# Optimization experiments

Measured on AMD Instinct MI355X. Metric: run time of the kernel, lower is better.

The kernel has to match this reference:

```python
import jax, jax.numpy as jnp
import numpy as np

EPS = 1e-5  # torch BatchNorm2d default


def _conv5x5(x, w, b):
    # x: [N,1,H,W], w: [1,1,5,5], b: [1]; stride 1, padding 2 (SAME)
    out = jax.lax.conv_general_dilated(
        x, w, window_strides=(1, 1), padding=((2, 2), (2, 2)),
        dimension_numbers=("NCHW", "OIHW", "NCHW"))
    return out + b[None, :, None, None]


def _batchnorm(x, gamma, beta):
    # training-mode BatchNorm2d: per-channel batch stats over (N,H,W), biased var
    mean = jnp.mean(x, axis=(0, 2, 3), keepdims=True)
    var = jnp.mean(jnp.square(x - mean), axis=(0, 2, 3), keepdims=True)
    xhat = (x - mean) * jax.lax.rsqrt(var + EPS)
    return xhat * gamma[None, :, None, None] + beta[None, :, None, None]


def _shrinkage(x, lumdb):
    return x + 0.5 * (jnp.sqrt(jnp.square(x - lumdb) + 1.0)
                      - jnp.sqrt(jnp.square(x + lumdb) + 1.0))


def setup_inputs() -> dict:
    key = jax.random.key(0)
    k1, k2, k3 = jax.random.split(key, 3)
    y = jax.random.normal(k1, (64, 1, 512, 512), dtype=jnp.float32)
    # kaiming-uniform-ish init for a 1x1x5x5 conv
    fan_in = 25.0
    bound = 1.0 / np.sqrt(fan_in)
    conv_w = jax.random.uniform(k2, (1, 1, 5, 5), jnp.float32, -bound, bound)
    conv_b = jax.random.uniform(k3, (1,), jnp.float32, -bound, bound)
    gamma = jnp.ones((1,), jnp.float32)
    beta = jnp.zeros((1,), jnp.float32)
    lambd = jnp.array([2.0, 1.0, 0.0], jnp.float32)
    return {"y": y, "conv_w": conv_w, "conv_b": conv_b,
            "gamma": gamma, "beta": beta, "lambd": lambd}


def reference(y, conv_w, conv_b, gamma, beta, lambd):
    x_k = y
    # unrolled LISTA iteration 1
    x = _batchnorm(_conv5x5(x_k, conv_w, conv_b), gamma, beta)
    x = _shrinkage(x, lambd[0])
    o12 = _batchnorm(_conv5x5(x, conv_w, conv_b), gamma, beta)
    x = _batchnorm(_conv5x5(x_k, conv_w, conv_b), gamma, beta)
    # iteration 2
    x = _shrinkage(o12 + x, lambd[1])
    o22 = _batchnorm(_conv5x5(x, conv_w, conv_b), gamma, beta)
    x = _batchnorm(_conv5x5(x_k, conv_w, conv_b), gamma, beta)
    # iteration 3
    x = _shrinkage(o22 + x, lambd[2])
    return x
```

## Files before the change

### kernel.cpp

```cpp
#include <hip/hip_runtime.h>
#include <math.h>

#define HH 512
#define WW 512
#define NTOT (64u*512u*512u)
#define NBLK 1024
#define TS 128
#define TROWS 132
#define TCH 18
#define TPIT 152
#define NTASK (TROWS*TCH)
#define NITER 10

typedef __attribute__((ext_vector_type(8))) short short8;
typedef __attribute__((ext_vector_type(4))) float f32x4;

__device__ __forceinline__ float fsqrtf(float x) { return __builtin_amdgcn_sqrtf(x); }

__device__ __forceinline__ float shrinkf(float x, float l) {
    float a = x - l, b = x + l;
    return x + 0.5f * (fsqrtf(__builtin_fmaf(a, a, 1.f)) - fsqrtf(__builtin_fmaf(b, b, 1.f)));
}

__device__ __forceinline__ float bf2f(unsigned int u) {
    union { unsigned int i; float f; } cv;
    cv.i = u << 16;
    return cv.f;
}
__device__ __forceinline__ float lo2f(unsigned int p) {
    union { unsigned int i; float f; } cv; cv.i = p << 16; return cv.f;
}
__device__ __forceinline__ float hi2f(unsigned int p) {
    union { unsigned int i; float f; } cv; cv.i = p & 0xffff0000u; return cv.f;
}

__device__ __forceinline__ unsigned int cvtpk(float lo, float hi) {
    unsigned int r;
    asm("v_cvt_pk_bf16_f32 %0, %1, %2" : "=v"(r) : "v"(lo), "v"(hi));
    return r;
}

__device__ __forceinline__ void bf8(uint4 u, float* f) {
    f[0] = bf2f(u.x & 0xffffu); f[1] = bf2f(u.x >> 16);
    f[2] = bf2f(u.y & 0xffffu); f[3] = bf2f(u.y >> 16);
    f[4] = bf2f(u.z & 0xffffu); f[5] = bf2f(u.z >> 16);
    f[6] = bf2f(u.w & 0xffffu); f[7] = bf2f(u.w >> 16);
}

template <int MODE, bool OBF>
__global__ __launch_bounds__(256, 4) void conv_k(
    const float* __restrict__ yin,
    const unsigned short* __restrict__ t1,
    const unsigned short* __restrict__ t2,
    unsigned short* __restrict__ outbf,
    float* __restrict__ outf32,
    const float* __restrict__ wgt,
    const float* __restrict__ bias,
    const float* __restrict__ stats,
    const float* __restrict__ lambd,
    float* __restrict__ partials)
{
    __shared__ unsigned short tile[TROWS * TPIT];

    const int tid = threadIdx.x;
    const int by = blockIdx.y * TS;
    const int bx = blockIdx.x * TS;
    const size_t ibase = (size_t)blockIdx.z * (HH * WW);

    float s1 = 0.f, h1 = 0.f, s2v = 0.f, h2 = 0.f, lam = 0.f;
    if constexpr (MODE == 1) { s1 = stats[0]; h1 = stats[1]; lam = lambd[0]; }
    if constexpr (MODE == 2) {
        s1 = stats[0]; h1 = stats[1]; s2v = stats[2]; h2 = stats[3]; lam = lambd[1];
    }

    float wloc[25];
#pragma unroll
    for (int i = 0; i < 25; i++) wloc[i] = wgt[i];

    const int lane = tid & 63;
    const int lm = lane & 15;
    const int kb = lane >> 4;
    const int basei = kb * 8 - lm - 6;
    short8 bfr[5];
#pragma unroll
    for (int ky = 0; ky < 5; ky++) {
        unsigned pkw[4];
#pragma unroll
        for (int jj = 0; jj < 4; jj++) {
            float v0 = 0.f, v1 = 0.f;
            const int i0 = basei + 2 * jj, i1 = i0 + 1;
#pragma unroll
            for (int t = 0; t < 5; t++) {
                if (i0 == t) v0 = wloc[ky * 5 + t];
                if (i1 == t) v1 = wloc[ky * 5 + t];
            }
            pkw[jj] = cvtpk(v0, v1);
        }
        union { unsigned u[4]; short8 s; } cv;
        cv.u[0] = pkw[0]; cv.u[1] = pkw[1]; cv.u[2] = pkw[2]; cv.u[3] = pkw[3];
        bfr[ky] = cv.s;
    }

    auto loadT = [&](int task, uint4& A, uint4& B) {
        A = make_uint4(0u,0u,0u,0u); B = make_uint4(0u,0u,0u,0u);
        const int row = task / TCH;
        const int ch  = task - row * TCH;
        const int gy  = by + row - 2;
        const int gx0 = bx + ch * 8 - 8;
        if (task < NTASK && gy >= 0 && gy < HH && gx0 >= 0 && gx0 <= WW - 8) {
            const size_t g = ibase + (size_t)gy * WW + gx0;
            if constexpr (MODE == 0) {
                A = *(const uint4*)(yin + g);
                B = *(const uint4*)(yin + g + 4);
            } else if constexpr (MODE == 1) {
                A = *(const uint4*)(t1 + g);
            } else {
                A = *(const uint4*)(t1 + g);
                B = *(const uint4*)(t2 + g);
            }
        }
    };

    auto procT = [&](int task, uint4 A, uint4 B) {
        const int row = task / TCH;
        const int ch  = task - row * TCH;
        uint4 pk = make_uint4(0u,0u,0u,0u);
        if constexpr (MODE == 0) {
            const float4 a = *(const float4*)&A;
            const float4 b = *(const float4*)&B;
            pk.x = cvtpk(a.x, a.y); pk.y = cvtpk(a.z, a.w);
            pk.z = cvtpk(b.x, b.y); pk.w = cvtpk(b.z, b.w);
        } else if constexpr (MODE == 1) {
            float f1[8]; bf8(A, f1);
            float v[8];
#pragma unroll
            for (int k = 0; k < 8; k++)
                v[k] = shrinkf(__builtin_fmaf(f1[k], s1, h1), lam);
            pk.x = cvtpk(v[0], v[1]); pk.y = cvtpk(v[2], v[3]);
            pk.z = cvtpk(v[4], v[5]); pk.w = cvtpk(v[6], v[7]);
        } else {
            float f1[8], f2[8]; bf8(A, f1); bf8(B, f2);
            float v[8];
#pragma unroll
            for (int k = 0; k < 8; k++) {
                float x = __builtin_fmaf(f2[k], s2v, h2)
                        + __builtin_fmaf(f1[k], s1, h1);
                v[k] = shrinkf(x, lam);
            }
            pk.x = cvtpk(v[0], v[1]); pk.y = cvtpk(v[2], v[3]);
            pk.z = cvtpk(v[4], v[5]); pk.w = cvtpk(v[6], v[7]);
        }
        const int gy  = by + row - 2;
        const int gx0 = bx + ch * 8 - 8;
        if (!(gy >= 0 && gy < HH && gx0 >= 0 && gx0 <= WW - 8))
            pk = make_uint4(0u,0u,0u,0u);
        *(uint4*)&tile[row * TPIT + ch * 8] = pk;
    };

    uint4 sA0, sB0, sA1, sB1, sA2, sB2;
    loadT(tid,        sA0, sB0);
    loadT(tid + 256,  sA1, sB1);
    loadT(tid + 512,  sA2, sB2);
#pragma unroll
    for (int t = 0; t < NITER; t++) {
        const int task = tid + t * 256;
        if (task < NTASK) procT(task, sA0, sB0);
        sA0 = sA1; sB0 = sB1;
        sA1 = sA2; sB1 = sB2;
        if (t + 3 < NITER) {
            loadT(tid + (t + 3) * 256, sA2, sB2);
        } else {
            sA2 = make_uint4(0u,0u,0u,0u); sB2 = make_uint4(0u,0u,0u,0u);
        }
    }

    const float b0 = bias[0];
    __syncthreads();

    const int wv = tid >> 6;
    const int r0w = wv * 32;

    f32x4 acc[2][8];
#pragma unroll
    for (int st = 0; st < 2; st++)
#pragma unroll
        for (int ct = 0; ct < 8; ct++)
            acc[st][ct] = (f32x4){0.f, 0.f, 0.f, 0.f};

#pragma unroll
    for (int ky = 0; ky < 5; ky++) {
        const short8 b = bfr[ky];
#pragma unroll
        for (int st = 0; st < 2; st++) {
            const unsigned short* ab = &tile[(r0w + st * 16 + lm + ky) * TPIT + kb * 8];
#pragma unroll
            for (int ct = 0; ct < 8; ct++) {
                short8 a = *(const short8*)(ab + ct * 16);
                acc[st][ct] = __builtin_amdgcn_mfma_f32_16x16x32_bf16(a, b, acc[st][ct], 0, 0, 0);
            }
        }
    }

    float s = 0.f, q = 0.f;
#pragma unroll
    for (int st = 0; st < 2; st++) {
#pragma unroll
        for (int ct = 0; ct < 8; ct++) {
            const f32x4 a = acc[st][ct];
            const int grow0 = by + r0w + st * 16 + kb * 4;
            const size_t base = ibase + (size_t)grow0 * WW + bx + ct * 16 + lm;
            if constexpr (OBF) {
                unsigned p01 = cvtpk(a[0] + b0, a[1] + b0);
                unsigned p23 = cvtpk(a[2] + b0, a[3] + b0);
                outbf[base]          = (unsigned short)(p01 & 0xffffu);
                outbf[base + WW]     = (unsigned short)(p01 >> 16);
                outbf[base + 2 * WW] = (unsigned short)(p23 & 0xffffu);
                outbf[base + 3 * WW] = (unsigned short)(p23 >> 16);
                float fr0 = lo2f(p01), fr1 = hi2f(p01), fr2 = lo2f(p23), fr3 = hi2f(p23);
                s += fr0 + fr1 + fr2 + fr3;
                q = __builtin_fmaf(fr0, fr0, __builtin_fmaf(fr1, fr1,
                    __builtin_fmaf(fr2, fr2, __builtin_fmaf(fr3, fr3, q))));
            } else {
                float f0 = a[0] + b0, f1v = a[1] + b0, f2v = a[2] + b0, f3v = a[3] + b0;
                outf32[base]          = f0;
                outf32[base + WW]     = f1v;
                outf32[base + 2 * WW] = f2v;
                outf32[base + 3 * WW] = f3v;
                s += f0 + f1v + f2v + f3v;
                q = __builtin_fmaf(f0, f0, __builtin_fmaf(f1v, f1v,
                    __builtin_fmaf(f2v, f2v, __builtin_fmaf(f3v, f3v, q))));
            }
        }
    }

    __syncthreads();
    float* red = (float*)tile;
    red[tid] = s; red[256 + tid] = q;
    __syncthreads();
    for (int off = 128; off > 0; off >>= 1) {
        if (tid < off) { red[tid] += red[tid + off]; red[256 + tid] += red[256 + tid + off]; }
        __syncthreads();
    }
    if (tid == 0) {
        const int bid = (blockIdx.z * 4 + blockIdx.y) * 4 + blockIdx.x;
        partials[bid * 2] = red[0];
        partials[bid * 2 + 1] = red[256];
    }
}

__global__ __launch_bounds__(256) void finalize_k(
    const float* __restrict__ partials, float* __restrict__ stats, int stage,
    const float* __restrict__ gamma, const float* __restrict__ beta)
{
    __shared__ double rs[256], rq[256];
    const int tid = threadIdx.x;
    double s = 0.0, q = 0.0;
    for (int i = tid; i < NBLK; i += 256) { s += partials[2 * i]; q += partials[2 * i + 1]; }
    rs[tid] = s; rq[tid] = q;
    __syncthreads();
    for (int off = 128; off > 0; off >>= 1) {
        if (tid < off) { rs[tid] += rs[tid + off]; rq[tid] += rq[tid + off]; }
        __syncthreads();
    }
    if (tid == 0) {
        double mean = rs[0] / (double)NTOT;
        double var = rq[0] / (double)NTOT - mean * mean;
        double scl = (double)gamma[0] / sqrt(var + 1e-5);
        stats[2 * stage] = (float)scl;
        stats[2 * stage + 1] = (float)((double)beta[0] - mean * scl);
    }
}

template <bool T3BF>
__global__ __launch_bounds__(256) void final_k(
    const unsigned short* __restrict__ t1,
    const unsigned short* __restrict__ t3b,
    float* __restrict__ io,
    const float* __restrict__ stats, const float* __restrict__ lambd)
{
    const float s1 = stats[0], h1 = stats[1], s3 = stats[4], h3 = stats[5];
    const float lam = lambd[2];
    const size_t base = ((size_t)blockIdx.x * 256 + threadIdx.x) * 8;

    uint4 u1 = *(const uint4*)(t1 + base);
    float f1[8]; bf8(u1, f1);

    float t3v[8];
    if constexpr (T3BF) {
        uint4 u3 = *(const uint4*)(t3b + base);
        bf8(u3, t3v);
    } else {
        float4 a0 = *(const float4*)(io + base);
        float4 a1 = *(const float4*)(io + base + 4);
        t3v[0]=a0.x; t3v[1]=a0.y; t3v[2]=a0.z; t3v[3]=a0.w;
        t3v[4]=a1.x; t3v[5]=a1.y; t3v[6]=a1.z; t3v[7]=a1.w;
    }

    float r[8];
#pragma unroll
    for (int k = 0; k < 8; k++) {
        float v = __builtin_fmaf(t3v[k], s3, h3) + __builtin_fmaf(f1[k], s1, h1);
        r[k] = shrinkf(v, lam);
    }
    *(float4*)(io + base)     = make_float4(r[0], r[1], r[2], r[3]);
    *(float4*)(io + base + 4) = make_float4(r[4], r[5], r[6], r[7]);
}

extern "C" void kernel_launch(void* const* d_in, const int* in_sizes, int n_in,
                              void* d_out, int out_size, void* d_ws, size_t ws_size,
                              hipStream_t stream)
{
    const float* y     = (const float*)d_in[0];
    const float* wgt   = (const float*)d_in[1];
    const float* bias  = (const float*)d_in[2];
    const float* gamma = (const float*)d_in[3];
    const float* beta  = (const float*)d_in[4];
    const float* lambd = (const float*)d_in[5];
    float* out = (float*)d_out;

    char* ws = (char*)d_ws;
    unsigned short* t1 = (unsigned short*)ws;
    unsigned short* t2 = (unsigned short*)(ws + 33554432ull);
    unsigned short* t3 = (unsigned short*)(ws + 67108864ull);
    const bool t3bf = (ws_size >= 100696088ull);
    const size_t poff = t3bf ? 100663296ull : 67108864ull;
    float* partials = (float*)(ws + poff);
    float* stats    = (float*)(ws + poff + 32768ull);

    dim3 grid(4, 4, 64), blk(256);
    conv_k<0, true><<<grid, blk, 0, stream>>>(y, nullptr, nullptr, t1, nullptr,
                                              wgt, bias, stats, lambd, partials);
    finalize_k<<<1, blk, 0, stream>>>(partials, stats, 0, gamma, beta);
    conv_k<1, true><<<grid, blk, 0, stream>>>(nullptr, t1, nullptr, t2, nullptr,
                                              wgt, bias, stats, lambd, partials);
    finalize_k<<<1, blk, 0, stream>>>(partials, stats, 1, gamma, beta);
    if (t3bf) {
        conv_k<2, true><<<grid, blk, 0, stream>>>(nullptr, t1, t2, t3, nullptr,
                                                  wgt, bias, stats, lambd, partials);
        finalize_k<<<1, blk, 0, stream>>>(partials, stats, 2, gamma, beta);
        final_k<true><<<8192, blk, 0, stream>>>(t1, t3, out, stats, lambd);
    } else {
        conv_k<2, false><<<grid, blk, 0, stream>>>(nullptr, t1, t2, nullptr, out,
                                                   wgt, bias, stats, lambd, partials);
        finalize_k<<<1, blk, 0, stream>>>(partials, stats, 2, gamma, beta);
        final_k<false><<<8192, blk, 0, stream>>>(t1, nullptr, out, stats, lambd);
    }
}
```

Measured before the change: 106.7 us.

## Fold BatchNorm stats finalization into consumer kernels, drop finalize launches

Removes the three single-block finalize kernels by having every block of the next conv (and the final elementwise kernel) redundantly reduce the 1024 per-block partials into scale/shift in double precision. The prefetch loads of the input tile are issued before this reduction so global-load latency overlaps it. Partials for each stage now live in separate buffers so they are not overwritten while still needed. The final kernel is resized to 1024 blocks each handling 8 chunks, which amortizes the redundant reduction. The cost is extra per-block reduction work and syncs, in exchange for fewer launches and serialization gaps.

After: 97.84 us. -8.3%, faster.

```diff
diff --git a/kernel.cpp b/kernel.cpp
--- a/kernel.cpp
+++ b/kernel.cpp
@@ -47,6 +47,31 @@
     f[6] = bf2f(u.w & 0xffffu); f[7] = bf2f(u.w >> 16);
 }
 
+__device__ __forceinline__ void stats_reduce(
+    const float* __restrict__ part, double* rs, double* rq, int tid,
+    float gam, float bet, float& scl_out, float& shf_out)
+{
+    double sd = 0.0, qd = 0.0;
+#pragma unroll
+    for (int k = 0; k < 4; k++) {
+        const int i = tid + k * 256;
+        sd += (double)part[2 * i];
+        qd += (double)part[2 * i + 1];
+    }
+    rs[tid] = sd; rq[tid] = qd;
+    __syncthreads();
+    for (int off = 128; off > 0; off >>= 1) {
+        if (tid < off) { rs[tid] += rs[tid + off]; rq[tid] += rq[tid + off]; }
+        __syncthreads();
+    }
+    const double mean = rs[0] / (double)NTOT;
+    const double var  = rq[0] / (double)NTOT - mean * mean;
+    const double scl  = (double)gam / sqrt(var + 1e-5);
+    scl_out = (float)scl;
+    shf_out = (float)((double)bet - mean * scl);
+    __syncthreads();
+}
+
 template <int MODE, bool OBF>
 __global__ __launch_bounds__(256, 4) void conv_k(
     const float* __restrict__ yin,
@@ -56,7 +81,11 @@
     float* __restrict__ outf32,
     const float* __restrict__ wgt,
     const float* __restrict__ bias,
-    const float* __restrict__ stats,
+    const float* __restrict__ prevPart,
+    const float* __restrict__ statsIn,
+    float* __restrict__ statsOut,
+    const float* __restrict__ gamma,
+    const float* __restrict__ beta,
     const float* __restrict__ lambd,
     float* __restrict__ partials)
 {
@@ -66,12 +95,6 @@
     const int by = blockIdx.y * TS;
     const int bx = blockIdx.x * TS;
     const size_t ibase = (size_t)blockIdx.z * (HH * WW);
-
-    float s1 = 0.f, h1 = 0.f, s2v = 0.f, h2 = 0.f, lam = 0.f;
-    if constexpr (MODE == 1) { s1 = stats[0]; h1 = stats[1]; lam = lambd[0]; }
-    if constexpr (MODE == 2) {
-        s1 = stats[0]; h1 = stats[1]; s2v = stats[2]; h2 = stats[3]; lam = lambd[1];
-    }
 
     float wloc[25];
 #pragma unroll
@@ -121,6 +144,27 @@
         }
     };
 
+    uint4 sA0, sB0, sA1, sB1, sA2, sB2;
+    loadT(tid,        sA0, sB0);
+    loadT(tid + 256,  sA1, sB1);
+    loadT(tid + 512,  sA2, sB2);
+
+    float s1 = 0.f, h1 = 0.f, s2v = 0.f, h2 = 0.f, lam = 0.f;
+    if constexpr (MODE == 1) {
+        stats_reduce(prevPart, (double*)tile, ((double*)tile) + 256, tid,
+                     gamma[0], beta[0], s1, h1);
+        lam = lambd[0];
+        if (tid == 0 && blockIdx.x == 0 && blockIdx.y == 0 && blockIdx.z == 0) {
+            statsOut[0] = s1; statsOut[1] = h1;
+        }
+    }
+    if constexpr (MODE == 2) {
+        stats_reduce(prevPart, (double*)tile, ((double*)tile) + 256, tid,
+                     gamma[0], beta[0], s2v, h2);
+        s1 = statsIn[0]; h1 = statsIn[1];
+        lam = lambd[1];
+    }
+
     auto procT = [&](int task, uint4 A, uint4 B) {
         const int row = task / TCH;
         const int ch  = task - row * TCH;
@@ -157,10 +201,6 @@
         *(uint4*)&tile[row * TPIT + ch * 8] = pk;
     };
 
-    uint4 sA0, sB0, sA1, sB1, sA2, sB2;
-    loadT(tid,        sA0, sB0);
-    loadT(tid + 256,  sA1, sB1);
-    loadT(tid + 512,  sA2, sB2);
 #pragma unroll
     for (int t = 0; t < NITER; t++) {
         const int task = tid + t * 256;
@@ -248,62 +288,53 @@
     }
 }
 
-__global__ __launch_bounds__(256) void finalize_k(
-    const float* __restrict__ partials, float* __restrict__ stats, int stage,
-    const float* __restrict__ gamma, const float* __restrict__ beta)
-{
-    __shared__ double rs[256], rq[256];
-    const int tid = threadIdx.x;
-    double s = 0.0, q = 0.0;
-    for (int i = tid; i < NBLK; i += 256) { s += partials[2 * i]; q += partials[2 * i + 1]; }
-    rs[tid] = s; rq[tid] = q;
-    __syncthreads();
-    for (int off = 128; off > 0; off >>= 1) {
-        if (tid < off) { rs[tid] += rs[tid + off]; rq[tid] += rq[tid + off]; }
-        __syncthreads();
-    }
-    if (tid == 0) {
-        double mean = rs[0] / (double)NTOT;
-        double var = rq[0] / (double)NTOT - mean * mean;
-        double scl = (double)gamma[0] / sqrt(var + 1e-5);
-        stats[2 * stage] = (float)scl;
-        stats[2 * stage + 1] = (float)((double)beta[0] - mean * scl);
-    }
-}
-
 template <bool T3BF>
 __global__ __launch_bounds__(256) void final_k(
     const unsigned short* __restrict__ t1,
     const unsigned short* __restrict__ t3b,
     float* __restrict__ io,
-    const float* __restrict__ stats, const float* __restrict__ lambd)
+    const float* __restrict__ p3,
+    const float* __restrict__ statsIn,
+    const float* __restrict__ gamma,
+    const float* __restrict__ beta,
+    const float* __restrict__ lambd)
 {
-    const float s1 = stats[0], h1 = stats[1], s3 = stats[4], h3 = stats[5];
+    __shared__ double rbuf[512];
+    const int tid = threadIdx.x;
+
+    float s3, h3;
+    stats_reduce(p3, rbuf, rbuf + 256, tid, gamma[0], beta[0], s3, h3);
+    const float s1 = statsIn[0], h1 = statsIn[1];
     const float lam = lambd[2];
-    const size_t base = ((size_t)blockIdx.x * 256 + threadIdx.x) * 8;
-
-    uint4 u1 = *(const uint4*)(t1 + base);
-    float f1[8]; bf8(u1, f1);
-
-    float t3v[8];
-    if constexpr (T3BF) {
-        uint4 u3 = *(const uint4*)(t3b + base);
-        bf8(u3, t3v);
-    } else {
-        float4 a0 = *(const float4*)(io + base);
-        float4 a1 = *(const float4*)(io + base + 4);
-        t3v[0]=a0.x; t3v[1]=a0.y; t3v[2]=a0.z; t3v[3]=a0.w;
-        t3v[4]=a1.x; t3v[5]=a1.y; t3v[6]=a1.z; t3v[7]=a1.w;
-    }
-
-    float r[8];
-#pragma unroll
-    for (int k = 0; k < 8; k++) {
-        float v = __builtin_fmaf(t3v[k], s3, h3) + __builtin_fmaf(f1[k], s1, h1);
-        r[k] = shrinkf(v, lam);
-    }
-    *(float4*)(io + base)     = make_float4(r[0], r[1], r[2], r[3]);
-    *(float4*)(io + base + 4) = make_float4(r[4], r[5], r[6], r[7]);
+
+#pragma unroll
+    for (int c = 0; c < 8; c++) {
+        const size_t idx = ((size_t)c * 1024 + blockIdx.x) * 256 + tid;
+        const size_t base = idx * 8;
+
+        uint4 u1 = *(const uint4*)(t1 + base);
+        float f1[8]; bf8(u1, f1);
+
+        float t3v[8];
+        if constexpr (T3BF) {
+            uint4 u3 = *(const uint4*)(t3b + base);
+            bf8(u3, t3v);
+        } else {
+            float4 a0 = *(const float4*)(io + base);
+            float4 a1 = *(const float4*)(io + base + 4);
+            t3v[0]=a0.x; t3v[1]=a0.y; t3v[2]=a0.z; t3v[3]=a0.w;
+            t3v[4]=a1.x; t3v[5]=a1.y; t3v[6]=a1.z; t3v[7]=a1.w;
+        }
+
+        float r[8];
+#pragma unroll
+        for (int k = 0; k < 8; k++) {
+            float v = __builtin_fmaf(t3v[k], s3, h3) + __builtin_fmaf(f1[k], s1, h1);
+            r[k] = shrinkf(v, lam);
+        }
+        *(float4*)(io + base)     = make_float4(r[0], r[1], r[2], r[3]);
+        *(float4*)(io + base + 4) = make_float4(r[4], r[5], r[6], r[7]);
+    }
 }
 
 extern "C" void kernel_launch(void* const* d_in, const int* in_sizes, int n_in,
@@ -324,25 +355,29 @@
     unsigned short* t3 = (unsigned short*)(ws + 67108864ull);
     const bool t3bf = (ws_size >= 100696088ull);
     const size_t poff = t3bf ? 100663296ull : 67108864ull;
-    float* partials = (float*)(ws + poff);
-    float* stats    = (float*)(ws + poff + 32768ull);
+    float* p1    = (float*)(ws + poff);
+    float* p2    = (float*)(ws + poff + 8192ull);
+    float* p3    = (float*)(ws + poff + 16384ull);
+    float* stats = (float*)(ws + poff + 24576ull);
 
     dim3 grid(4, 4, 64), blk(256);
     conv_k<0, true><<<grid, blk, 0, stream>>>(y, nullptr, nullptr, t1, nullptr,
-                                              wgt, bias, stats, lambd, partials);
-    finalize_k<<<1, blk, 0, stream>>>(partials, stats, 0, gamma, beta);
+                                              wgt, bias, nullptr, nullptr, nullptr,
+                                              gamma, beta, lambd, p1);
     conv_k<1, true><<<grid, blk, 0, stream>>>(nullptr, t1, nullptr, t2, nullptr,
-                                              wgt, bias, stats, lambd, partials);
-    finalize_k<<<1, blk, 0, stream>>>(partials, stats, 1, gamma, beta);
+                                              wgt, bias, p1, nullptr, stats,
+                                              gamma, beta, lambd, p2);
     if (t3bf) {
         conv_k<2, true><<<grid, blk, 0, stream>>>(nullptr, t1, t2, t3, nullptr,
-                                                  wgt, bias, stats, lambd, partials);
-        finalize_k<<<1, blk, 0, stream>>>(partials, stats, 2, gamma, beta);
-        final_k<true><<<8192, blk, 0, stream>>>(t1, t3, out, stats, lambd);
+                                                  wgt, bias, p2, stats, nullptr,
+                                                  gamma, beta, lambd, p3);
+        final_k<true><<<1024, blk, 0, stream>>>(t1, t3, out, p3, stats,
+                                                gamma, beta, lambd);
     } else {
         conv_k<2, false><<<grid, blk, 0, stream>>>(nullptr, t1, t2, nullptr, out,
-                                                   wgt, bias, stats, lambd, partials);
-        finalize_k<<<1, blk, 0, stream>>>(partials, stats, 2, gamma, beta);
-        final_k<false><<<8192, blk, 0, stream>>>(t1, nullptr, out, stats, lambd);
-    }
-}
+                                                   wgt, bias, p2, stats, nullptr,
+                                                   gamma, beta, lambd, p3);
+        final_k<false><<<1024, blk, 0, stream>>>(t1, nullptr, out, p3, stats,
+                                                 gamma, beta, lambd);
+    }
+}
```
